# Performance work log

Measured on AMD Instinct MI355X. Metric: run time of the kernel, lower is better.

The kernel has to match this reference:

```python
import jax, jax.numpy as jnp
import numpy as np

B, LATENT, HIDDEN, HEAD_H, OUT = 262144, 64, 512, 64, 4
EPS = 1e-5


def _layernorm(a, g, b):
    mu = jnp.mean(a, axis=-1, keepdims=True)
    var = jnp.mean(jnp.square(a - mu), axis=-1, keepdims=True)
    return (a - mu) / jnp.sqrt(var + EPS) * g + b


def _leaky(a):
    return jnp.where(a >= 0, a, 0.2 * a)


def setup_inputs() -> dict:
    key = jax.random.key(0)
    ks = jax.random.split(key, 12)
    s = lambda fan_in: 1.0 / np.sqrt(fan_in)
    return {
        "z": jax.random.normal(ks[0], (B, LATENT), dtype=jnp.float32),
        "x": jax.random.randint(ks[1], (B,), 0, 2, dtype=jnp.int32),
        "y": jax.random.randint(ks[2], (B,), 0, 2, dtype=jnp.int32),
        # encoder params (Linear stored as [in, out])
        "W1": jax.random.normal(ks[3], (LATENT, HIDDEN), dtype=jnp.float32) * s(LATENT),
        "b1": jnp.zeros((HIDDEN,), dtype=jnp.float32),
        "g1": jnp.ones((HIDDEN,), dtype=jnp.float32),
        "beta1": jnp.zeros((HIDDEN,), dtype=jnp.float32),
        "W2": jax.random.normal(ks[4], (HIDDEN, HIDDEN), dtype=jnp.float32) * s(HIDDEN),
        "b2": jnp.zeros((HIDDEN,), dtype=jnp.float32),
        "g2": jnp.ones((HIDDEN,), dtype=jnp.float32),
        "beta2": jnp.zeros((HIDDEN,), dtype=jnp.float32),
        # 4 setting-specific heads, stacked on leading axis k = 2*x + y
        "Wh1": jax.random.normal(ks[5], (4, HIDDEN, HEAD_H), dtype=jnp.float32) * s(HIDDEN),
        "bh1": jnp.zeros((4, HEAD_H), dtype=jnp.float32),
        "Wh2": jax.random.normal(ks[6], (4, HEAD_H, OUT), dtype=jnp.float32) * s(HEAD_H),
        "bh2": jnp.zeros((4, OUT), dtype=jnp.float32),
    }


def reference(z, x, y, W1, b1, g1, beta1, W2, b2, g2, beta2, Wh1, bh1, Wh2, bh2):
    # encoder: Linear -> LayerNorm -> LeakyReLU(0.2), twice
    h = _leaky(_layernorm(z @ W1 + b1, g1, beta1))          # [B, HIDDEN]
    h = _leaky(_layernorm(h @ W2 + b2, g2, beta2))          # [B, HIDDEN]
    # all 4 heads in one pass, then per-row select (equivalent to mask routing)
    t = jax.nn.relu(jnp.einsum("bh,khd->bkd", h, Wh1) + bh1)  # [B, 4, HEAD_H]
    logits_all = jnp.einsum("bkd,kdo->bko", t, Wh2) + bh2     # [B, 4, OUT]
    k = 2 * x + y                                              # head index per row
    logits = logits_all[jnp.arange(logits_all.shape[0]), k]    # [B, OUT]
    return jax.nn.softmax(logits, axis=-1)
```

## Files before the change

### kernel.cpp

```cpp
#include <hip/hip_runtime.h>

#define MT 48
#define TS 520
#define NROWS 262144
#define EPSV 1e-5f

typedef __attribute__((ext_vector_type(8))) short short8;
typedef __attribute__((ext_vector_type(4))) float floatx4;
typedef __attribute__((ext_vector_type(2))) float floatx2;
typedef __attribute__((ext_vector_type(4))) unsigned int uintx4;
typedef __attribute__((ext_vector_type(2))) unsigned int uintx2;

__device__ __forceinline__ unsigned short f2bf(float f) {
    unsigned u = __builtin_bit_cast(unsigned, f);
    u += 0x7fff + ((u >> 16) & 1);
    return (unsigned short)(u >> 16);
}
__device__ __forceinline__ float bf2f(short s) {
    unsigned u = ((unsigned)(unsigned short)s) << 16;
    return __builtin_bit_cast(float, u);
}
__device__ __forceinline__ unsigned cvtpk(float a, float b) {
    unsigned r;
    asm("v_cvt_pk_bf16_f32 %0, %1, %2" : "=v"(r) : "v"(a), "v"(b));
    return r;
}
__device__ __forceinline__ floatx2 pk_add(floatx2 a, floatx2 b) {
    floatx2 d; asm("v_pk_add_f32 %0, %1, %2" : "=v"(d) : "v"(a), "v"(b)); return d;
}
__device__ __forceinline__ floatx2 pk_mul(floatx2 a, floatx2 b) {
    floatx2 d; asm("v_pk_mul_f32 %0, %1, %2" : "=v"(d) : "v"(a), "v"(b)); return d;
}
__device__ __forceinline__ floatx2 pk_fma(floatx2 a, floatx2 b, floatx2 c) {
    floatx2 d; asm("v_pk_fma_f32 %0, %1, %2, %3" : "=v"(d) : "v"(a), "v"(b), "v"(c)); return d;
}
template<int C>
__device__ __forceinline__ float dpp_add(float v) {
    int t = __builtin_amdgcn_update_dpp(0, __builtin_bit_cast(int, v), C, 0xf, 0xf, true);
    return v + __builtin_bit_cast(float, t);
}
__device__ __forceinline__ float red16(float v) {
    v = dpp_add<0x111>(v);
    v = dpp_add<0x112>(v);
    v = dpp_add<0x114>(v);
    v = dpp_add<0x118>(v);
    return v;
}

__global__ void convert_weights(const float* __restrict__ W1, const float* __restrict__ W2,
                                const float* __restrict__ Wh1, short* __restrict__ ws) {
    int idx = blockIdx.x * 256 + threadIdx.x;
    if (idx < 32768) {
        int j = idx & 7, lane = (idx >> 3) & 63, c = idx >> 9;
        int ks = c & 1, nt = (c >> 1) & 7, w = c >> 4;
        int k = ks * 32 + (lane >> 4) * 8 + j;
        int n = w * 128 + nt * 16 + (lane & 15);
        ws[idx] = (short)f2bf(W1[k * 512 + n]);
    } else if (idx < 32768 + 262144) {
        int jdx = idx - 32768;
        int j = jdx & 7, lane = (jdx >> 3) & 63, c = jdx >> 9;
        int nt = c & 7, ks = (c >> 3) & 15, w = c >> 7;
        int kp = ks * 32 + (lane >> 4) * 8 + j;
        int k  = (kp & 0x180) + ((kp & 7) << 4) + ((kp >> 3) & 15);
        int n = w * 128 + nt * 16 + (lane & 15);
        ws[idx] = (short)f2bf(W2[k * 512 + n]);
    } else if (idx < 32768 + 262144 + 131072) {
        int jdx = idx - (32768 + 262144);
        int j = jdx & 7, lane = (jdx >> 3) & 63, c = jdx >> 9;
        int nt = c & 3, ks = (c >> 2) & 15, w = c >> 6;
        int kp = ks * 32 + (lane >> 4) * 8 + j;
        int k  = (kp & 0x180) + ((kp & 7) << 4) + ((kp >> 3) & 15);
        int col = w * 64 + nt * 16 + (lane & 15);
        int kk = col >> 6, d = col & 63;
        ws[idx] = (short)f2bf(Wh1[(kk * 512 + k) * 64 + d]);
    }
}

__global__ __launch_bounds__(256, 2) void fused_kernel(
    const float* __restrict__ z, const int* __restrict__ x, const int* __restrict__ y,
    const float* __restrict__ b1, const float* __restrict__ g1, const float* __restrict__ be1,
    const float* __restrict__ b2, const float* __restrict__ g2, const float* __restrict__ be2,
    const float* __restrict__ bh1, const float* __restrict__ Wh2, const float* __restrict__ bh2,
    const short* __restrict__ ws, float* __restrict__ out)
{
    __shared__ __align__(16) short tile[MT * TS];
    __shared__ float psum[4][MT];
    __shared__ float psq[4][MT];
    __shared__ float rmean[MT];
    __shared__ float rrstd[MT];

    int tid  = threadIdx.x;
    int wave = tid >> 6;
    int lane = tid & 63;
    int quad = lane >> 4;
    int l16  = lane & 15;
    int blk0 = blockIdx.x * MT;
    int nslab = wave * 128;

    const short* bbase1 = ws + wave * (16 * 512) + lane * 8;
    const short* bbase2 = ws + 32768 + wave * (16 * 8 * 512) + lane * 8;
    const short* bbase3 = ws + 32768 + 262144 + wave * (16 * 4 * 512) + lane * 8;

    floatx4 acc[3][8];
    short8 b2a[8], b2b[8];
    short8 b3a[4], b3b[4];

#pragma unroll
    for (int mt = 0; mt < 3; mt++)
#pragma unroll
        for (int nt = 0; nt < 8; nt++) acc[mt][nt] = (floatx4){0.f, 0.f, 0.f, 0.f};

    __builtin_amdgcn_s_setprio(1);
#pragma unroll
    for (int ks = 0; ks < 2; ks++) {
        short8 afr[3];
#pragma unroll
        for (int mt = 0; mt < 3; mt++) {
            int row = blk0 + mt * 16 + l16;
            row = (row < NROWS) ? row : (NROWS - 1);
            const float* zp = z + row * 64 + ks * 32 + quad * 8;
            floatx4 f0 = *(const floatx4*)zp;
            floatx4 f1 = *(const floatx4*)(zp + 4);
            uintx4 up;
            up[0] = cvtpk(f0[0], f0[1]); up[1] = cvtpk(f0[2], f0[3]);
            up[2] = cvtpk(f1[0], f1[1]); up[3] = cvtpk(f1[2], f1[3]);
            afr[mt] = __builtin_bit_cast(short8, up);
        }
#pragma unroll
        for (int nt = 0; nt < 8; nt++) {
            short8 b = *(const short8*)(bbase1 + (nt * 2 + ks) * 512);
#pragma unroll
            for (int mt = 0; mt < 3; mt++)
                acc[mt][nt] = __builtin_amdgcn_mfma_f32_16x16x32_bf16(afr[mt], b, acc[mt][nt], 0, 0, 0);
        }
    }
    __builtin_amdgcn_s_setprio(0);

#pragma unroll
    for (int nt = 0; nt < 8; nt++) b2a[nt] = *(const short8*)(bbase2 + nt * 512);

    {
        floatx2 s2[3][2] = {}, q2[3][2] = {};
#pragma unroll
        for (int nt = 0; nt < 8; nt++) {
            float bv = b1[nslab + nt * 16 + l16];
            floatx2 bb = {bv, bv};
#pragma unroll
            for (int mt = 0; mt < 3; mt++) {
                floatx2 v01 = {acc[mt][nt][0], acc[mt][nt][1]};
                floatx2 v23 = {acc[mt][nt][2], acc[mt][nt][3]};
                v01 = pk_add(v01, bb); v23 = pk_add(v23, bb);
                acc[mt][nt][0] = v01[0]; acc[mt][nt][1] = v01[1];
                acc[mt][nt][2] = v23[0]; acc[mt][nt][3] = v23[1];
                s2[mt][0] = pk_add(s2[mt][0], v01); q2[mt][0] = pk_fma(v01, v01, q2[mt][0]);
                s2[mt][1] = pk_add(s2[mt][1], v23); q2[mt][1] = pk_fma(v23, v23, q2[mt][1]);
            }
        }
#pragma unroll
        for (int mt = 0; mt < 3; mt++)
#pragma unroll
            for (int pr = 0; pr < 2; pr++) {
                s2[mt][pr][0] = red16(s2[mt][pr][0]); s2[mt][pr][1] = red16(s2[mt][pr][1]);
                q2[mt][pr][0] = red16(q2[mt][pr][0]); q2[mt][pr][1] = red16(q2[mt][pr][1]);
            }
        if (l16 == 15) {
#pragma unroll
            for (int mt = 0; mt < 3; mt++)
#pragma unroll
                for (int pr = 0; pr < 2; pr++) {
                    int row = mt * 16 + quad * 4 + pr * 2;
                    *(floatx2*)&psum[wave][row] = s2[mt][pr];
                    *(floatx2*)&psq[wave][row]  = q2[mt][pr];
                }
        }
    }
    __syncthreads();
    if (tid < MT) {
        float s = psum[0][tid] + psum[1][tid] + psum[2][tid] + psum[3][tid];
        float q = psq[0][tid] + psq[1][tid] + psq[2][tid] + psq[3][tid];
        float mean = s * (1.f / 512.f);
        float var  = q * (1.f / 512.f) - mean * mean;
        rmean[tid] = -mean;
        rrstd[tid] = rsqrtf(var + EPSV);
    }
    __syncthreads();
    {
        floatx2 nm[3][2], rs[3][2];
#pragma unroll
        for (int mt = 0; mt < 3; mt++)
#pragma unroll
            for (int pr = 0; pr < 2; pr++) {
                int row = mt * 16 + quad * 4 + pr * 2;
                nm[mt][pr] = *(const floatx2*)&rmean[row];
                rs[mt][pr] = *(const floatx2*)&rrstd[row];
            }
        floatx2 ggA[8], bbA[8];
#pragma unroll
        for (int nt = 0; nt < 8; nt++) {
            int col = nslab + nt * 16 + l16;
            float g = g1[col], be = be1[col];
            ggA[nt] = (floatx2){g, g}; bbA[nt] = (floatx2){be, be};
        }
#pragma unroll
        for (int mt = 0; mt < 3; mt++)
#pragma unroll
            for (int pr = 0; pr < 2; pr++) {
                float fa[8], fb[8];
#pragma unroll
                for (int nt = 0; nt < 8; nt++) {
                    floatx2 v = {acc[mt][nt][2 * pr], acc[mt][nt][2 * pr + 1]};
                    floatx2 t = pk_mul(pk_add(v, nm[mt][pr]), rs[mt][pr]);
                    floatx2 f = pk_fma(t, ggA[nt], bbA[nt]);
                    fa[nt] = fmaxf(f[0], 0.2f * f[0]);
                    fb[nt] = fmaxf(f[1], 0.2f * f[1]);
                }
                int row = mt * 16 + quad * 4 + pr * 2;
                uintx4 ua, ub;
                ua[0] = cvtpk(fa[0], fa[1]); ua[1] = cvtpk(fa[2], fa[3]);
                ua[2] = cvtpk(fa[4], fa[5]); ua[3] = cvtpk(fa[6], fa[7]);
                ub[0] = cvtpk(fb[0], fb[1]); ub[1] = cvtpk(fb[2], fb[3]);
                ub[2] = cvtpk(fb[4], fb[5]); ub[3] = cvtpk(fb[6], fb[7]);
                *(uintx4*)&tile[row * TS + nslab + l16 * 8]       = ua;
                *(uintx4*)&tile[(row + 1) * TS + nslab + l16 * 8] = ub;
            }
    }
    __syncthreads();

#pragma unroll
    for (int mt = 0; mt < 3; mt++)
#pragma unroll
        for (int nt = 0; nt < 8; nt++) acc[mt][nt] = (floatx4){0.f, 0.f, 0.f, 0.f};

    __builtin_amdgcn_s_setprio(1);
#pragma unroll
    for (int ks = 0; ks < 16; ks += 2) {
#pragma unroll
        for (int nt = 0; nt < 8; nt++)
            b2b[nt] = *(const short8*)(bbase2 + ((ks + 1) * 8 + nt) * 512);
        {
            short8 afr[3];
#pragma unroll
            for (int mt = 0; mt < 3; mt++)
                afr[mt] = *(const short8*)&tile[(mt * 16 + l16) * TS + ks * 32 + quad * 8];
#pragma unroll
            for (int nt = 0; nt < 8; nt++)
#pragma unroll
                for (int mt = 0; mt < 3; mt++)
                    acc[mt][nt] = __builtin_amdgcn_mfma_f32_16x16x32_bf16(afr[mt], b2a[nt], acc[mt][nt], 0, 0, 0);
        }
        if (ks + 2 < 16) {
#pragma unroll
            for (int nt = 0; nt < 8; nt++)
                b2a[nt] = *(const short8*)(bbase2 + ((ks + 2) * 8 + nt) * 512);
        }
        {
            short8 afr[3];
#pragma unroll
            for (int mt = 0; mt < 3; mt++)
                afr[mt] = *(const short8*)&tile[(mt * 16 + l16) * TS + (ks + 1) * 32 + quad * 8];
#pragma unroll
            for (int nt = 0; nt < 8; nt++)
#pragma unroll
                for (int mt = 0; mt < 3; mt++)
                    acc[mt][nt] = __builtin_amdgcn_mfma_f32_16x16x32_bf16(afr[mt], b2b[nt], acc[mt][nt], 0, 0, 0);
        }
    }
    __builtin_amdgcn_s_setprio(0);

#pragma unroll
    for (int nt = 0; nt < 4; nt++) b3a[nt] = *(const short8*)(bbase3 + nt * 512);

    {
        floatx2 s2[3][2] = {}, q2[3][2] = {};
#pragma unroll
        for (int nt = 0; nt < 8; nt++) {
            float bv = b2[nslab + nt * 16 + l16];
            floatx2 bb = {bv, bv};
#pragma unroll
            for (int mt = 0; mt < 3; mt++) {
                floatx2 v01 = {acc[mt][nt][0], acc[mt][nt][1]};
                floatx2 v23 = {acc[mt][nt][2], acc[mt][nt][3]};
                v01 = pk_add(v01, bb); v23 = pk_add(v23, bb);
                acc[mt][nt][0] = v01[0]; acc[mt][nt][1] = v01[1];
                acc[mt][nt][2] = v23[0]; acc[mt][nt][3] = v23[1];
                s2[mt][0] = pk_add(s2[mt][0], v01); q2[mt][0] = pk_fma(v01, v01, q2[mt][0]);
                s2[mt][1] = pk_add(s2[mt][1], v23); q2[mt][1] = pk_fma(v23, v23, q2[mt][1]);
            }
        }
#pragma unroll
        for (int mt = 0; mt < 3; mt++)
#pragma unroll
            for (int pr = 0; pr < 2; pr++) {
                s2[mt][pr][0] = red16(s2[mt][pr][0]); s2[mt][pr][1] = red16(s2[mt][pr][1]);
                q2[mt][pr][0] = red16(q2[mt][pr][0]); q2[mt][pr][1] = red16(q2[mt][pr][1]);
            }
        if (l16 == 15) {
#pragma unroll
            for (int mt = 0; mt < 3; mt++)
#pragma unroll
                for (int pr = 0; pr < 2; pr++) {
                    int row = mt * 16 + quad * 4 + pr * 2;
                    *(floatx2*)&psum[wave][row] = s2[mt][pr];
                    *(floatx2*)&psq[wave][row]  = q2[mt][pr];
                }
        }
    }
    __syncthreads();
    if (tid < MT) {
        float s = psum[0][tid] + psum[1][tid] + psum[2][tid] + psum[3][tid];
        float q = psq[0][tid] + psq[1][tid] + psq[2][tid] + psq[3][tid];
        float mean = s * (1.f / 512.f);
        float var  = q * (1.f / 512.f) - mean * mean;
        rmean[tid] = -mean;
        rrstd[tid] = rsqrtf(var + EPSV);
    }
    __syncthreads();
    {
        floatx2 nm[3][2], rs[3][2];
#pragma unroll
        for (int mt = 0; mt < 3; mt++)
#pragma unroll
            for (int pr = 0; pr < 2; pr++) {
                int row = mt * 16 + quad * 4 + pr * 2;
                nm[mt][pr] = *(const floatx2*)&rmean[row];
                rs[mt][pr] = *(const floatx2*)&rrstd[row];
            }
        floatx2 ggA[8], bbA[8];
#pragma unroll
        for (int nt = 0; nt < 8; nt++) {
            int col = nslab + nt * 16 + l16;
            float g = g2[col], be = be2[col];
            ggA[nt] = (floatx2){g, g}; bbA[nt] = (floatx2){be, be};
        }
#pragma unroll
        for (int mt = 0; mt < 3; mt++)
#pragma unroll
            for (int pr = 0; pr < 2; pr++) {
                float fa[8], fb[8];
#pragma unroll
                for (int nt = 0; nt < 8; nt++) {
                    floatx2 v = {acc[mt][nt][2 * pr], acc[mt][nt][2 * pr + 1]};
                    floatx2 t = pk_mul(pk_add(v, nm[mt][pr]), rs[mt][pr]);
                    floatx2 f = pk_fma(t, ggA[nt], bbA[nt]);
                    fa[nt] = fmaxf(f[0], 0.2f * f[0]);
                    fb[nt] = fmaxf(f[1], 0.2f * f[1]);
                }
                int row = mt * 16 + quad * 4 + pr * 2;
                uintx4 ua, ub;
                ua[0] = cvtpk(fa[0], fa[1]); ua[1] = cvtpk(fa[2], fa[3]);
                ua[2] = cvtpk(fa[4], fa[5]); ua[3] = cvtpk(fa[6], fa[7]);
                ub[0] = cvtpk(fb[0], fb[1]); ub[1] = cvtpk(fb[2], fb[3]);
                ub[2] = cvtpk(fb[4], fb[5]); ub[3] = cvtpk(fb[6], fb[7]);
                *(uintx4*)&tile[row * TS + nslab + l16 * 8]       = ua;
                *(uintx4*)&tile[(row + 1) * TS + nslab + l16 * 8] = ub;
            }
    }
    __syncthreads();

#pragma unroll
    for (int mt = 0; mt < 3; mt++)
#pragma unroll
        for (int nt = 0; nt < 4; nt++) acc[mt][nt] = (floatx4){0.f, 0.f, 0.f, 0.f};

    __builtin_amdgcn_s_setprio(1);
#pragma unroll
    for (int ks = 0; ks < 16; ks += 2) {
#pragma unroll
        for (int nt = 0; nt < 4; nt++)
            b3b[nt] = *(const short8*)(bbase3 + ((ks + 1) * 4 + nt) * 512);
        {
            short8 afr[3];
#pragma unroll
            for (int mt = 0; mt < 3; mt++)
                afr[mt] = *(const short8*)&tile[(mt * 16 + l16) * TS + ks * 32 + quad * 8];
#pragma unroll
            for (int nt = 0; nt < 4; nt++)
#pragma unroll
                for (int mt = 0; mt < 3; mt++)
                    acc[mt][nt] = __builtin_amdgcn_mfma_f32_16x16x32_bf16(afr[mt], b3a[nt], acc[mt][nt], 0, 0, 0);
        }
        if (ks + 2 < 16) {
#pragma unroll
            for (int nt = 0; nt < 4; nt++)
                b3a[nt] = *(const short8*)(bbase3 + ((ks + 2) * 4 + nt) * 512);
        }
        {
            short8 afr[3];
#pragma unroll
            for (int mt = 0; mt < 3; mt++)
                afr[mt] = *(const short8*)&tile[(mt * 16 + l16) * TS + (ks + 1) * 32 + quad * 8];
#pragma unroll
            for (int nt = 0; nt < 4; nt++)
#pragma unroll
                for (int mt = 0; mt < 3; mt++)
                    acc[mt][nt] = __builtin_amdgcn_mfma_f32_16x16x32_bf16(afr[mt], b3b[nt], acc[mt][nt], 0, 0, 0);
        }
    }
    __builtin_amdgcn_s_setprio(0);
    __syncthreads();
    {
        float bh1v[4];
#pragma unroll
        for (int nt = 0; nt < 4; nt++) bh1v[nt] = bh1[wave * 64 + nt * 16 + l16];
#pragma unroll
        for (int mt = 0; mt < 3; mt++)
#pragma unroll
            for (int r2 = 0; r2 < 4; r2++) {
                int row = mt * 16 + quad * 4 + r2;
                float f[4];
#pragma unroll
                for (int nt = 0; nt < 4; nt++) {
                    float v = acc[mt][nt][r2] + bh1v[nt];
                    f[nt] = (v > 0.f) ? v : 0.f;
                }
                uintx2 up = {cvtpk(f[0], f[1]), cvtpk(f[2], f[3])};
                *(uintx2*)&tile[row * TS + wave * 64 + l16 * 4] = up;
            }
    }
    __syncthreads();

    {
        int r = tid >> 2, is = tid & 3;
        if (r < MT) {
            int grow = blk0 + r;
            int gsafe = (grow < NROWS) ? grow : (NROWS - 1);
            int kk = 2 * x[gsafe] + y[gsafe];
            const short* tp = &tile[r * TS + kk * 64 + is * 16];
            short8 ta = *(const short8*)tp;
            short8 tb = *(const short8*)(tp + 8);
            const float* wp = Wh2 + kk * 256;
            float lg0 = 0.f, lg1 = 0.f, lg2 = 0.f, lg3 = 0.f;
#pragma unroll
            for (int e = 0; e < 8; e++) {
                int d0 = (e & 3) * 16 + 4 * is + (e >> 2);
                float t0 = bf2f(ta[e]);
                floatx4 w0 = *(const floatx4*)(wp + d0 * 4);
                float t1 = bf2f(tb[e]);
                floatx4 w1 = *(const floatx4*)(wp + (d0 + 2) * 4);
                lg0 += t0 * w0[0] + t1 * w1[0];
                lg1 += t0 * w0[1] + t1 * w1[1];
                lg2 += t0 * w0[2] + t1 * w1[2];
                lg3 += t0 * w0[3] + t1 * w1[3];
            }
#pragma unroll
            for (int off = 1; off < 4; off <<= 1) {
                lg0 += __shfl_xor(lg0, off, 64);
                lg1 += __shfl_xor(lg1, off, 64);
                lg2 += __shfl_xor(lg2, off, 64);
                lg3 += __shfl_xor(lg3, off, 64);
            }
            if (is == 0 && grow < NROWS) {
                lg0 += bh2[kk * 4 + 0]; lg1 += bh2[kk * 4 + 1];
                lg2 += bh2[kk * 4 + 2]; lg3 += bh2[kk * 4 + 3];
                float m = fmaxf(fmaxf(lg0, lg1), fmaxf(lg2, lg3));
                float e0 = __expf(lg0 - m), e1 = __expf(lg1 - m);
                float e2 = __expf(lg2 - m), e3 = __expf(lg3 - m);
                float inv = 1.f / (e0 + e1 + e2 + e3);
                floatx4 o = {e0 * inv, e1 * inv, e2 * inv, e3 * inv};
                *(floatx4*)(out + grow * 4) = o;
            }
        }
    }
}

extern "C" void kernel_launch(void* const* d_in, const int* in_sizes, int n_in,
                              void* d_out, int out_size, void* d_ws, size_t ws_size,
                              hipStream_t stream) {
    const float* z   = (const float*)d_in[0];
    const int*   x   = (const int*)d_in[1];
    const int*   y   = (const int*)d_in[2];
    const float* W1  = (const float*)d_in[3];
    const float* b1  = (const float*)d_in[4];
    const float* g1  = (const float*)d_in[5];
    const float* be1 = (const float*)d_in[6];
    const float* W2  = (const float*)d_in[7];
    const float* b2  = (const float*)d_in[8];
    const float* g2  = (const float*)d_in[9];
    const float* be2 = (const float*)d_in[10];
    const float* Wh1 = (const float*)d_in[11];
    const float* bh1 = (const float*)d_in[12];
    const float* Wh2 = (const float*)d_in[13];
    const float* bh2 = (const float*)d_in[14];
    short* ws = (short*)d_ws;
    float* out = (float*)d_out;

    hipLaunchKernelGGL(convert_weights, dim3(1664), dim3(256), 0, stream, W1, W2, Wh1, ws);
    hipLaunchKernelGGL(fused_kernel, dim3((NROWS + MT - 1) / MT), dim3(256), 0, stream,
                       z, x, y, b1, g1, be1, b2, g2, be2, bh1, Wh2, bh2,
                       (const short*)ws, out);
}
```

Baseline: 436.3 us.

## Raise row tile to 64 and drop manual weight double-buffering in GEMM loops

Increases rows per block from 48 to 64 (4 M-subtiles per wave), so each weight fragment loaded from global memory feeds more MFMAs and fewer blocks are launched. Because 64 divides the row count evenly, the bounds clamps and tail guards are removed. The explicit b2a/b2b and b3a/b3b register double-buffering of weight fragments is replaced with simple per-k loads, leaving latency hiding to the compiler. This frees registers for the larger accumulator set, but risks exposed global-load latency and more LDS use per block, which may lower occupancy.

```diff
diff --git a/kernel.cpp b/kernel.cpp
--- a/kernel.cpp
+++ b/kernel.cpp
@@ -1,6 +1,7 @@
 #include <hip/hip_runtime.h>
 
-#define MT 48
+#define MT 64
+#define MTM 4
 #define TS 520
 #define NROWS 262144
 #define EPSV 1e-5f
@@ -101,23 +102,20 @@
     const short* bbase2 = ws + 32768 + wave * (16 * 8 * 512) + lane * 8;
     const short* bbase3 = ws + 32768 + 262144 + wave * (16 * 4 * 512) + lane * 8;
 
-    floatx4 acc[3][8];
-    short8 b2a[8], b2b[8];
-    short8 b3a[4], b3b[4];
-
-#pragma unroll
-    for (int mt = 0; mt < 3; mt++)
+    floatx4 acc[MTM][8];
+
+#pragma unroll
+    for (int mt = 0; mt < MTM; mt++)
 #pragma unroll
         for (int nt = 0; nt < 8; nt++) acc[mt][nt] = (floatx4){0.f, 0.f, 0.f, 0.f};
 
     __builtin_amdgcn_s_setprio(1);
 #pragma unroll
     for (int ks = 0; ks < 2; ks++) {
-        short8 afr[3];
-#pragma unroll
-        for (int mt = 0; mt < 3; mt++) {
+        short8 afr[MTM];
+#pragma unroll
+        for (int mt = 0; mt < MTM; mt++) {
             int row = blk0 + mt * 16 + l16;
-            row = (row < NROWS) ? row : (NROWS - 1);
             const float* zp = z + row * 64 + ks * 32 + quad * 8;
             floatx4 f0 = *(const floatx4*)zp;
             floatx4 f1 = *(const floatx4*)(zp + 4);
@@ -130,23 +128,20 @@
         for (int nt = 0; nt < 8; nt++) {
             short8 b = *(const short8*)(bbase1 + (nt * 2 + ks) * 512);
 #pragma unroll
-            for (int mt = 0; mt < 3; mt++)
+            for (int mt = 0; mt < MTM; mt++)
                 acc[mt][nt] = __builtin_amdgcn_mfma_f32_16x16x32_bf16(afr[mt], b, acc[mt][nt], 0, 0, 0);
         }
     }
     __builtin_amdgcn_s_setprio(0);
 
-#pragma unroll
-    for (int nt = 0; nt < 8; nt++) b2a[nt] = *(const short8*)(bbase2 + nt * 512);
-
-    {
-        floatx2 s2[3][2] = {}, q2[3][2] = {};
+    {
+        floatx2 s2[MTM][2] = {}, q2[MTM][2] = {};
 #pragma unroll
         for (int nt = 0; nt < 8; nt++) {
             float bv = b1[nslab + nt * 16 + l16];
             floatx2 bb = {bv, bv};
 #pragma unroll
-            for (int mt = 0; mt < 3; mt++) {
+            for (int mt = 0; mt < MTM; mt++) {
                 floatx2 v01 = {acc[mt][nt][0], acc[mt][nt][1]};
                 floatx2 v23 = {acc[mt][nt][2], acc[mt][nt][3]};
                 v01 = pk_add(v01, bb); v23 = pk_add(v23, bb);
@@ -157,7 +152,7 @@
             }
         }
 #pragma unroll
-        for (int mt = 0; mt < 3; mt++)
+        for (int mt = 0; mt < MTM; mt++)
 #pragma unroll
             for (int pr = 0; pr < 2; pr++) {
                 s2[mt][pr][0] = red16(s2[mt][pr][0]); s2[mt][pr][1] = red16(s2[mt][pr][1]);
@@ -165,7 +160,7 @@
             }
         if (l16 == 15) {
 #pragma unroll
-            for (int mt = 0; mt < 3; mt++)
+            for (int mt = 0; mt < MTM; mt++)
 #pragma unroll
                 for (int pr = 0; pr < 2; pr++) {
                     int row = mt * 16 + quad * 4 + pr * 2;
@@ -185,9 +180,9 @@
     }
     __syncthreads();
     {
-        floatx2 nm[3][2], rs[3][2];
-#pragma unroll
-        for (int mt = 0; mt < 3; mt++)
+        floatx2 nm[MTM][2], rs[MTM][2];
+#pragma unroll
+        for (int mt = 0; mt < MTM; mt++)
 #pragma unroll
             for (int pr = 0; pr < 2; pr++) {
                 int row = mt * 16 + quad * 4 + pr * 2;
@@ -202,7 +197,7 @@
             ggA[nt] = (floatx2){g, g}; bbA[nt] = (floatx2){be, be};
         }
 #pragma unroll
-        for (int mt = 0; mt < 3; mt++)
+        for (int mt = 0; mt < MTM; mt++)
 #pragma unroll
             for (int pr = 0; pr < 2; pr++) {
                 float fa[8], fb[8];
@@ -227,57 +222,33 @@
     __syncthreads();
 
 #pragma unroll
-    for (int mt = 0; mt < 3; mt++)
+    for (int mt = 0; mt < MTM; mt++)
 #pragma unroll
         for (int nt = 0; nt < 8; nt++) acc[mt][nt] = (floatx4){0.f, 0.f, 0.f, 0.f};
 
     __builtin_amdgcn_s_setprio(1);
-#pragma unroll
-    for (int ks = 0; ks < 16; ks += 2) {
-#pragma unroll
-        for (int nt = 0; nt < 8; nt++)
-            b2b[nt] = *(const short8*)(bbase2 + ((ks + 1) * 8 + nt) * 512);
-        {
-            short8 afr[3];
-#pragma unroll
-            for (int mt = 0; mt < 3; mt++)
-                afr[mt] = *(const short8*)&tile[(mt * 16 + l16) * TS + ks * 32 + quad * 8];
-#pragma unroll
-            for (int nt = 0; nt < 8; nt++)
-#pragma unroll
-                for (int mt = 0; mt < 3; mt++)
-                    acc[mt][nt] = __builtin_amdgcn_mfma_f32_16x16x32_bf16(afr[mt], b2a[nt], acc[mt][nt], 0, 0, 0);
-        }
-        if (ks + 2 < 16) {
-#pragma unroll
-            for (int nt = 0; nt < 8; nt++)
-                b2a[nt] = *(const short8*)(bbase2 + ((ks + 2) * 8 + nt) * 512);
-        }
-        {
-            short8 afr[3];
-#pragma unroll
-            for (int mt = 0; mt < 3; mt++)
-                afr[mt] = *(const short8*)&tile[(mt * 16 + l16) * TS + (ks + 1) * 32 + quad * 8];
-#pragma unroll
-            for (int nt = 0; nt < 8; nt++)
-#pragma unroll
-                for (int mt = 0; mt < 3; mt++)
-                    acc[mt][nt] = __builtin_amdgcn_mfma_f32_16x16x32_bf16(afr[mt], b2b[nt], acc[mt][nt], 0, 0, 0);
+    for (int ks = 0; ks < 16; ks++) {
+        short8 afr[MTM];
+#pragma unroll
+        for (int mt = 0; mt < MTM; mt++)
+            afr[mt] = *(const short8*)&tile[(mt * 16 + l16) * TS + ks * 32 + quad * 8];
+#pragma unroll
+        for (int nt = 0; nt < 8; nt++) {
+            short8 b = *(const short8*)(bbase2 + (ks * 8 + nt) * 512);
+#pragma unroll
+            for (int mt = 0; mt < MTM; mt++)
+                acc[mt][nt] = __builtin_amdgcn_mfma_f32_16x16x32_bf16(afr[mt], b, acc[mt][nt], 0, 0, 0);
         }
     }
     __builtin_amdgcn_s_setprio(0);
-
-#pragma unroll
-    for (int nt = 0; nt < 4; nt++) b3a[nt] = *(const short8*)(bbase3 + nt * 512);
-
-    {
-        floatx2 s2[3][2] = {}, q2[3][2] = {};
+    {
+        floatx2 s2[MTM][2] = {}, q2[MTM][2] = {};
 #pragma unroll
         for (int nt = 0; nt < 8; nt++) {
             float bv = b2[nslab + nt * 16 + l16];
             floatx2 bb = {bv, bv};
 #pragma unroll
-            for (int mt = 0; mt < 3; mt++) {
+            for (int mt = 0; mt < MTM; mt++) {
                 floatx2 v01 = {acc[mt][nt][0], acc[mt][nt][1]};
                 floatx2 v23 = {acc[mt][nt][2], acc[mt][nt][3]};
                 v01 = pk_add(v01, bb); v23 = pk_add(v23, bb);
@@ -288,7 +259,7 @@
             }
         }
 #pragma unroll
-        for (int mt = 0; mt < 3; mt++)
+        for (int mt = 0; mt < MTM; mt++)
 #pragma unroll
             for (int pr = 0; pr < 2; pr++) {
                 s2[mt][pr][0] = red16(s2[mt][pr][0]); s2[mt][pr][1] = red16(s2[mt][pr][1]);
@@ -296,7 +267,7 @@
             }
         if (l16 == 15) {
 #pragma unroll
-            for (int mt = 0; mt < 3; mt++)
+            for (int mt = 0; mt < MTM; mt++)
 #pragma unroll
                 for (int pr = 0; pr < 2; pr++) {
                     int row = mt * 16 + quad * 4 + pr * 2;
@@ -316,9 +287,9 @@
     }
     __syncthreads();
     {
-        floatx2 nm[3][2], rs[3][2];
-#pragma unroll
-        for (int mt = 0; mt < 3; mt++)
+        floatx2 nm[MTM][2], rs[MTM][2];
+#pragma unroll
+        for (int mt = 0; mt < MTM; mt++)
 #pragma unroll
             for (int pr = 0; pr < 2; pr++) {
                 int row = mt * 16 + quad * 4 + pr * 2;
@@ -333,7 +304,7 @@
             ggA[nt] = (floatx2){g, g}; bbA[nt] = (floatx2){be, be};
         }
 #pragma unroll
-        for (int mt = 0; mt < 3; mt++)
+        for (int mt = 0; mt < MTM; mt++)
 #pragma unroll
             for (int pr = 0; pr < 2; pr++) {
                 float fa[8], fb[8];
@@ -358,42 +329,22 @@
     __syncthreads();
 
 #pragma unroll
-    for (int mt = 0; mt < 3; mt++)
+    for (int mt = 0; mt < MTM; mt++)
 #pragma unroll
         for (int nt = 0; nt < 4; nt++) acc[mt][nt] = (floatx4){0.f, 0.f, 0.f, 0.f};
 
     __builtin_amdgcn_s_setprio(1);
-#pragma unroll
-    for (int ks = 0; ks < 16; ks += 2) {
-#pragma unroll
-        for (int nt = 0; nt < 4; nt++)
-            b3b[nt] = *(const short8*)(bbase3 + ((ks + 1) * 4 + nt) * 512);
-        {
-            short8 afr[3];
-#pragma unroll
-            for (int mt = 0; mt < 3; mt++)
-                afr[mt] = *(const short8*)&tile[(mt * 16 + l16) * TS + ks * 32 + quad * 8];
-#pragma unroll
-            for (int nt = 0; nt < 4; nt++)
-#pragma unroll
-                for (int mt = 0; mt < 3; mt++)
-                    acc[mt][nt] = __builtin_amdgcn_mfma_f32_16x16x32_bf16(afr[mt], b3a[nt], acc[mt][nt], 0, 0, 0);
-        }
-        if (ks + 2 < 16) {
-#pragma unroll
-            for (int nt = 0; nt < 4; nt++)
-                b3a[nt] = *(const short8*)(bbase3 + ((ks + 2) * 4 + nt) * 512);
-        }
-        {
-            short8 afr[3];
-#pragma unroll
-            for (int mt = 0; mt < 3; mt++)
-                afr[mt] = *(const short8*)&tile[(mt * 16 + l16) * TS + (ks + 1) * 32 + quad * 8];
-#pragma unroll
-            for (int nt = 0; nt < 4; nt++)
-#pragma unroll
-                for (int mt = 0; mt < 3; mt++)
-                    acc[mt][nt] = __builtin_amdgcn_mfma_f32_16x16x32_bf16(afr[mt], b3b[nt], acc[mt][nt], 0, 0, 0);
+    for (int ks = 0; ks < 16; ks++) {
+        short8 afr[MTM];
+#pragma unroll
+        for (int mt = 0; mt < MTM; mt++)
+            afr[mt] = *(const short8*)&tile[(mt * 16 + l16) * TS + ks * 32 + quad * 8];
+#pragma unroll
+        for (int nt = 0; nt < 4; nt++) {
+            short8 b = *(const short8*)(bbase3 + (ks * 4 + nt) * 512);
+#pragma unroll
+            for (int mt = 0; mt < MTM; mt++)
+                acc[mt][nt] = __builtin_amdgcn_mfma_f32_16x16x32_bf16(afr[mt], b, acc[mt][nt], 0, 0, 0);
         }
     }
     __builtin_amdgcn_s_setprio(0);
@@ -403,7 +354,7 @@
 #pragma unroll
         for (int nt = 0; nt < 4; nt++) bh1v[nt] = bh1[wave * 64 + nt * 16 + l16];
 #pragma unroll
-        for (int mt = 0; mt < 3; mt++)
+        for (int mt = 0; mt < MTM; mt++)
 #pragma unroll
             for (int r2 = 0; r2 < 4; r2++) {
                 int row = mt * 16 + quad * 4 + r2;
@@ -421,44 +372,41 @@
 
     {
         int r = tid >> 2, is = tid & 3;
-        if (r < MT) {
-            int grow = blk0 + r;
-            int gsafe = (grow < NROWS) ? grow : (NROWS - 1);
-            int kk = 2 * x[gsafe] + y[gsafe];
-            const short* tp = &tile[r * TS + kk * 64 + is * 16];
-            short8 ta = *(const short8*)tp;
-            short8 tb = *(const short8*)(tp + 8);
-            const float* wp = Wh2 + kk * 256;
-            float lg0 = 0.f, lg1 = 0.f, lg2 = 0.f, lg3 = 0.f;
-#pragma unroll
-            for (int e = 0; e < 8; e++) {
-                int d0 = (e & 3) * 16 + 4 * is + (e >> 2);
-                float t0 = bf2f(ta[e]);
-                floatx4 w0 = *(const floatx4*)(wp + d0 * 4);
-                float t1 = bf2f(tb[e]);
-                floatx4 w1 = *(const floatx4*)(wp + (d0 + 2) * 4);
-                lg0 += t0 * w0[0] + t1 * w1[0];
-                lg1 += t0 * w0[1] + t1 * w1[1];
-                lg2 += t0 * w0[2] + t1 * w1[2];
-                lg3 += t0 * w0[3] + t1 * w1[3];
-            }
-#pragma unroll
-            for (int off = 1; off < 4; off <<= 1) {
-                lg0 += __shfl_xor(lg0, off, 64);
-                lg1 += __shfl_xor(lg1, off, 64);
-                lg2 += __shfl_xor(lg2, off, 64);
-                lg3 += __shfl_xor(lg3, off, 64);
-            }
-            if (is == 0 && grow < NROWS) {
-                lg0 += bh2[kk * 4 + 0]; lg1 += bh2[kk * 4 + 1];
-                lg2 += bh2[kk * 4 + 2]; lg3 += bh2[kk * 4 + 3];
-                float m = fmaxf(fmaxf(lg0, lg1), fmaxf(lg2, lg3));
-                float e0 = __expf(lg0 - m), e1 = __expf(lg1 - m);
-                float e2 = __expf(lg2 - m), e3 = __expf(lg3 - m);
-                float inv = 1.f / (e0 + e1 + e2 + e3);
-                floatx4 o = {e0 * inv, e1 * inv, e2 * inv, e3 * inv};
-                *(floatx4*)(out + grow * 4) = o;
-            }
+        int grow = blk0 + r;
+        int kk = 2 * x[grow] + y[grow];
+        const short* tp = &tile[r * TS + kk * 64 + is * 16];
+        short8 ta = *(const short8*)tp;
+        short8 tb = *(const short8*)(tp + 8);
+        const float* wp = Wh2 + kk * 256;
+        float lg0 = 0.f, lg1 = 0.f, lg2 = 0.f, lg3 = 0.f;
+#pragma unroll
+        for (int e = 0; e < 8; e++) {
+            int d0 = (e & 3) * 16 + 4 * is + (e >> 2);
+            float t0 = bf2f(ta[e]);
+            floatx4 w0 = *(const floatx4*)(wp + d0 * 4);
+            float t1 = bf2f(tb[e]);
+            floatx4 w1 = *(const floatx4*)(wp + (d0 + 2) * 4);
+            lg0 += t0 * w0[0] + t1 * w1[0];
+            lg1 += t0 * w0[1] + t1 * w1[1];
+            lg2 += t0 * w0[2] + t1 * w1[2];
+            lg3 += t0 * w0[3] + t1 * w1[3];
+        }
+#pragma unroll
+        for (int off = 1; off < 4; off <<= 1) {
+            lg0 += __shfl_xor(lg0, off, 64);
+            lg1 += __shfl_xor(lg1, off, 64);
+            lg2 += __shfl_xor(lg2, off, 64);
+            lg3 += __shfl_xor(lg3, off, 64);
+        }
+        if (is == 0) {
+            lg0 += bh2[kk * 4 + 0]; lg1 += bh2[kk * 4 + 1];
+            lg2 += bh2[kk * 4 + 2]; lg3 += bh2[kk * 4 + 3];
+            float m = fmaxf(fmaxf(lg0, lg1), fmaxf(lg2, lg3));
+            float e0 = __expf(lg0 - m), e1 = __expf(lg1 - m);
+            float e2 = __expf(lg2 - m), e3 = __expf(lg3 - m);
+            float inv = 1.f / (e0 + e1 + e2 + e3);
+            floatx4 o = {e0 * inv, e1 * inv, e2 * inv, e3 * inv};
+            *(floatx4*)(out + grow * 4) = o;
         }
     }
 }
@@ -485,7 +433,7 @@
     float* out = (float*)d_out;
 
     hipLaunchKernelGGL(convert_weights, dim3(1664), dim3(256), 0, stream, W1, W2, Wh1, ws);
-    hipLaunchKernelGGL(fused_kernel, dim3((NROWS + MT - 1) / MT), dim3(256), 0, stream,
+    hipLaunchKernelGGL(fused_kernel, dim3(NROWS / MT), dim3(256), 0, stream,
                        z, x, y, b1, g1, be1, b2, g2, be2, bh1, Wh2, bh2,
                        (const short*)ws, out);
 }
```

Result: faster. 364.0 us (-16.6%).
